# Performance work log

Hardware: AMD Instinct MI355X
Metric: run time of the kernel (lower is better)

## Reference

```python
import jax, jax.numpy as jnp
import numpy as np

ALPHA = 0.3          # triplet margin
LOSS_WEIGHT = 1.0
VALID_COST = 100.0   # chosen so all queries are valid (query2gt ~ U[0,1))
POS_T = 3            # pos_thresh
NEG_T = 30           # neg_thresh
EPS = 1e-6           # torch pairwise_distance eps


def setup_inputs() -> dict:
    key0 = jax.random.key(0)
    ks = jax.random.split(key0, 6)
    Nq, V, K, D, G = 2048, 6, 4096, 256, 64
    attn = jax.random.normal(ks[0], (Nq, V, K), dtype=jnp.float32)
    query2gt = jax.random.uniform(ks[1], (Nq, G), dtype=jnp.float32)  # min < VALID_COST always
    query = jax.random.normal(ks[2], (Nq, V, D), dtype=jnp.float32)
    key = jax.random.normal(ks[3], (K, V, D), dtype=jnp.float32)
    pos_idx = jax.random.randint(ks[4], (V * Nq,), 0, POS_T, dtype=jnp.int64 if jax.config.jax_enable_x64 else jnp.int32)
    neg_idx = jax.random.randint(ks[5], (V * Nq,), POS_T, NEG_T, dtype=jnp.int64 if jax.config.jax_enable_x64 else jnp.int32)
    return {"attn": attn, "query2gt": query2gt, "query": query, "key": key,
            "pos_idx": pos_idx, "neg_idx": neg_idx}


def reference(attn, query2gt, query, key, pos_idx, neg_idx):
    # valid filtering: query2gt.min(-1) < VALID_COST is all-True by construction,
    # so no rows are dropped (keeps shapes static under jit).
    q = jnp.transpose(query, (1, 0, 2))   # [V, Nq, D]
    k = jnp.transpose(key, (1, 0, 2))     # [V, K, D]
    a = jnp.transpose(attn, (1, 0, 2))    # [V, Nq, K]
    V, Nq, K = a.shape

    # batched euclidean cdist per view via gram expansion
    qq = jnp.sum(q * q, axis=-1)[:, :, None]          # [V, Nq, 1]
    kk = jnp.sum(k * k, axis=-1)[:, None, :]          # [V, 1, K]
    d2 = qq + kk - 2.0 * jnp.einsum('vnd,vkd->vnk', q, k)
    dist = jnp.sqrt(jnp.maximum(d2, 0.0))             # [V, Nq, K]

    sorted_idx = jnp.argsort(dist, axis=-1).reshape(V * Nq, K)
    a = a.reshape(V * Nq, K)
    r = jnp.arange(V * Nq)

    pos = jax.nn.sigmoid(a[r, sorted_idx[r, pos_idx]])  # [V*Nq]
    neg = jax.nn.sigmoid(a[r, sorted_idx[r, neg_idx]])  # [V*Nq]

    # TripletMarginLoss(margin=ALPHA, p=1) with anchor = ones, 1-d embeddings
    d_pos = jnp.abs(1.0 - pos + EPS)
    d_neg = jnp.abs(1.0 - neg + EPS)
    loss = jnp.mean(jnp.maximum(d_pos - d_neg + ALPHA, 0.0))
    return LOSS_WEIGHT * loss
```

## Files before the change

### kernel.cpp

```cpp
#include <hip/hip_runtime.h>
#include <stdint.h>

#define NQ    2048
#define VV    6
#define KCNT  4096
#define DD    256
#define NROWS (VV*NQ)
#define ALPHA_M 0.3f
#define EPSL  1e-6f
#define SBIAS 256.0f
#define ZTHR  2.05f
#define CAP   256

#define TM 128
#define TN 128
#define BKK 32

typedef _Float16 f16x8 __attribute__((ext_vector_type(8)));
typedef _Float16 f16x4 __attribute__((ext_vector_type(4)));
typedef float    f32x4 __attribute__((ext_vector_type(4)));

__device__ __forceinline__ void gload16(const void* g, void* l) {
    __builtin_amdgcn_global_load_lds(
        (__attribute__((address_space(1))) void*)(uintptr_t)g,
        (__attribute__((address_space(3))) void*)(uintptr_t)(uint32_t)(uintptr_t)l,
        16, 0, 0);
}

__device__ __forceinline__ unsigned ord16(_Float16 h) {
    unsigned short b = __builtin_bit_cast(unsigned short, h);
    return (b & 0x8000u) ? (unsigned)(~b & 0xFFFFu) : (unsigned)(b | 0x8000u);
}

__device__ __forceinline__ float triplet_term(const float* attn, int r, int kpos, int kneg) {
    int v = r / NQ, q = r - v * NQ;
    float apos = attn[(size_t)q * (VV*KCNT) + v*KCNT + kpos];
    float aneg = attn[(size_t)q * (VV*KCNT) + v*KCNT + kneg];
    float pv = 1.0f / (1.0f + expf(-apos));
    float nv = 1.0f / (1.0f + expf(-aneg));
    float dp = fabsf(1.0f - pv + EPSL);
    float dn = fabsf(1.0f - nv + EPSL);
    return fmaxf(dp - dn + ALPHA_M, 0.0f);
}

__global__ __launch_bounds__(256) void pack_fused(const float* __restrict__ key,
                                                  const float* __restrict__ query,
                                                  _Float16* __restrict__ Bpack,
                                                  _Float16* __restrict__ Apack,
                                                  float* __restrict__ kkp,
                                                  float* __restrict__ Trow,
                                                  unsigned* __restrict__ fcount,
                                                  float* __restrict__ out)
{
    int wid  = threadIdx.x >> 6;
    int lane = threadIdx.x & 63;
    if (blockIdx.x < 6144) {
        int rowid = blockIdx.x * 4 + wid;
        int k = rowid / 6;
        int v = rowid - k * 6;
        float4 x = *(const float4*)(key + (size_t)rowid * DD + lane * 4);
        f16x4 h;
        h.x = (_Float16)x.x; h.y = (_Float16)x.y;
        h.z = (_Float16)x.z; h.w = (_Float16)x.w;
        *(f16x4*)(Bpack + ((size_t)(v * KCNT + k)) * DD + lane * 4) = h;

        float s = x.x*x.x + x.y*x.y + x.z*x.z + x.w*x.w;
        #pragma unroll
        for (int off = 32; off >= 1; off >>= 1) s += __shfl_xor(s, off);
        if (lane == 0) kkp[v * KCNT + k] = s;
    } else {
        int bid2 = blockIdx.x - 6144;
        if (bid2 == 0) {
            if (threadIdx.x == 0) *fcount = 0;
            if (threadIdx.x == 1) out[0] = 0.0f;
        }
        int rowid = bid2 * 4 + wid;
        int q = rowid / 6;
        int v = rowid - q * 6;
        float4 x = *(const float4*)(query + (size_t)rowid * DD + lane * 4);
        f16x4 h;
        h.x = (_Float16)x.x; h.y = (_Float16)x.y;
        h.z = (_Float16)x.z; h.w = (_Float16)x.w;
        *(f16x4*)(Apack + ((size_t)(v * NQ + q)) * DD + lane * 4) = h;

        float qq = x.x*x.x + x.y*x.y + x.z*x.z + x.w*x.w;
        #pragma unroll
        for (int off = 32; off >= 1; off >>= 1) qq += __shfl_xor(qq, off);
        if (lane == 0)
            Trow[v * NQ + q] = 256.0f - ZTHR * sqrtf(512.0f + 4.0f * qq);
    }
}

__global__ __launch_bounds__(256) void score_gemm(const _Float16* __restrict__ Apack,
                                                  const _Float16* __restrict__ Bpack,
                                                  const float* __restrict__ kkp,
                                                  const float* __restrict__ Trow,
                                                  unsigned long long* __restrict__ maskb,
                                                  _Float16* __restrict__ wsf)
{
    __shared__ _Float16 As[TM * BKK];
    __shared__ _Float16 Bs[TN * BKK];

    int tid  = threadIdx.x;
    int wid  = tid >> 6;
    int lane = tid & 63;
    int c0   = blockIdx.x * TN;
    int grow = blockIdx.y * TM;
    int v    = grow / NQ;
    int q0   = grow - v * NQ;

    int srow = (wid << 4) + (lane >> 2);
    int sseg = (lane & 3) ^ ((lane >> 2) & 3);
    const _Float16* Ag0 = Apack + ((size_t)(v*NQ   + q0 + srow)) * DD + sseg*8;
    const _Float16* Ag1 = Ag0 + (size_t)64 * DD;
    const _Float16* Bg0 = Bpack + ((size_t)(v*KCNT + c0 + srow)) * DD + sseg*8;
    const _Float16* Bg1 = Bg0 + (size_t)64 * DD;

    _Float16* lA0 = As + wid*512;
    _Float16* lA1 = As + 2048 + wid*512;
    _Float16* lB0 = Bs + wid*512;
    _Float16* lB1 = Bs + 2048 + wid*512;

    int fr = lane & 15;
    int kg = lane >> 4;
    int rb = (wid >> 1) * 64;
    int cb = (wid & 1) * 64;
    int rg = lane >> 4;
    int ksw = (kg ^ (fr & 3)) << 3;

    f32x4 acc[4][4] = {};

    for (int kb = 0; kb < DD; kb += BKK) {
        __syncthreads();
        gload16(Ag0 + kb, lA0);
        gload16(Ag1 + kb, lA1);
        gload16(Bg0 + kb, lB0);
        gload16(Bg1 + kb, lB1);
        __syncthreads();

        f16x8 af[4], bf[4];
        #pragma unroll
        for (int m = 0; m < 4; ++m)
            af[m] = *(const f16x8*)&As[(rb + m*16 + fr)*BKK + ksw];
        #pragma unroll
        for (int n = 0; n < 4; ++n)
            bf[n] = *(const f16x8*)&Bs[(cb + n*16 + fr)*BKK + ksw];
        #pragma unroll
        for (int m = 0; m < 4; ++m)
            #pragma unroll
            for (int n = 0; n < 4; ++n)
                acc[m][n] = __builtin_amdgcn_mfma_f32_16x16x32_f16(af[m], bf[n], acc[m][n], 0, 0, 0);
    }

    int chunk = blockIdx.x * 2 + (wid & 1);
    float kkv[4];
    #pragma unroll
    for (int n = 0; n < 4; ++n)
        kkv[n] = kkp[v*KCNT + c0 + cb + n*16 + fr];

    int sh = rg * 16;

    #pragma unroll
    for (int m = 0; m < 4; ++m) {
        #pragma unroll
        for (int j = 0; j < 4; ++j) {
            int gr = grow + rb + m*16 + rg*4 + j;
            float Tr = Trow[gr];
            unsigned long long mk = 0;
            #pragma unroll
            for (int n = 0; n < 4; ++n) {
                float s = kkv[n] - 2.0f * acc[m][n][j];
                wsf[(size_t)gr * KCNT + (c0 + cb + n*16 + fr)] = (_Float16)(s - SBIAS);
                unsigned long long bal = __ballot(s < Tr);
                mk |= (unsigned long long)((unsigned)(bal >> sh) & 0xFFFFu) << (n*16);
            }
            if (fr == 0) maskb[((size_t)gr << 6) + chunk] = mk;
        }
    }
}

__global__ __launch_bounds__(256) void select2_kernel(const unsigned long long* __restrict__ maskb,
                                                      const _Float16* __restrict__ wsf,
                                                      const float* __restrict__ attn,
                                                      const int* __restrict__ pos_idx,
                                                      const int* __restrict__ neg_idx,
                                                      unsigned* __restrict__ fcount,
                                                      int* __restrict__ flist,
                                                      float* __restrict__ out)
{
    __shared__ unsigned cbuf[4][CAP];
    __shared__ float bsum;
    if (threadIdx.x == 0) bsum = 0.0f;
    __syncthreads();

    int wid  = threadIdx.x >> 6;
    int lane = threadIdx.x & 63;
    int r    = blockIdx.x * 4 + wid;
    int p = pos_idx[r];
    int n = neg_idx[r];

    unsigned long long mk = maskb[((size_t)r << 6) + lane];
    unsigned c_l = (unsigned)__popcll(mk);
    unsigned pre = c_l;
    #pragma unroll
    for (int off = 1; off <= 32; off <<= 1) {
        unsigned o = __shfl_up(pre, off);
        if (lane >= off) pre += o;
    }
    unsigned total = __shfl(pre, 63);
    unsigned excl  = pre - c_l;

    if (total < (unsigned)(n + 1) || total > CAP) {
        if (lane == 0) {
            unsigned i = atomicAdd(fcount, 1u);
            flist[i] = r;
        }
    } else {
        unsigned* mybuf = cbuf[wid];
        const _Float16* srow = wsf + (size_t)r * KCNT + (lane << 6);
        unsigned idx = excl;
        unsigned long long t = mk;
        while (t) {
            int b = __ffsll((long long)t) - 1;
            t &= t - 1;
            _Float16 h = srow[b];
            mybuf[idx++] = (ord16(h) << 12) | (unsigned)((lane << 6) + b);
        }
        __asm__ volatile("s_waitcnt lgkmcnt(0)" ::: "memory");

        unsigned v0 = (lane       < (int)total) ? mybuf[lane]       : 0xFFFFFFFFu;
        unsigned v1 = (lane + 64  < (int)total) ? mybuf[lane + 64]  : 0xFFFFFFFFu;
        unsigned v2 = (lane + 128 < (int)total) ? mybuf[lane + 128] : 0xFFFFFFFFu;
        unsigned v3 = (lane + 192 < (int)total) ? mybuf[lane + 192] : 0xFFFFFFFFu;
        int kpos = 0, kneg = 0;
        for (int t2 = 0; t2 <= n; ++t2) {
            unsigned m01 = v0 < v1 ? v0 : v1;
            unsigned m23 = v2 < v3 ? v2 : v3;
            unsigned m = m01 < m23 ? m01 : m23;
            #pragma unroll
            for (int off = 32; off >= 1; off >>= 1) {
                unsigned o = __shfl_xor(m, off);
                m = o < m ? o : m;
            }
            if      (v0 == m) v0 = 0xFFFFFFFFu;
            else if (v1 == m) v1 = 0xFFFFFFFFu;
            else if (v2 == m) v2 = 0xFFFFFFFFu;
            else if (v3 == m) v3 = 0xFFFFFFFFu;
            if (t2 == p) kpos = (int)(m & 0xFFFu);
            if (t2 == n) kneg = (int)(m & 0xFFFu);
        }
        if (lane == 0)
            atomicAdd(&bsum, triplet_term(attn, r, kpos, kneg) * (1.0f / (float)NROWS));
    }
    __syncthreads();
    if (threadIdx.x == 0) atomicAdd(out, bsum);
}

__global__ __launch_bounds__(256) void fallback_kernel(const _Float16* __restrict__ Apack,
                                                       const _Float16* __restrict__ Bpack,
                                                       const float* __restrict__ kkp,
                                                       const float* __restrict__ attn,
                                                       const int* __restrict__ pos_idx,
                                                       const int* __restrict__ neg_idx,
                                                       const unsigned* __restrict__ fcount,
                                                       const int* __restrict__ flist,
                                                       float* __restrict__ out)
{
    __shared__ float qrow[DD];
    __shared__ unsigned keys[KCNT];
    int nf = (int)*fcount;
    for (int it = blockIdx.x; it < nf; it += gridDim.x) {
        int r = flist[it];
        int v = r / NQ, q = r - v * NQ;
        qrow[threadIdx.x] = (float)Apack[((size_t)(v*NQ + q)) * DD + threadIdx.x];
        __syncthreads();
        for (int i = 0; i < 16; ++i) {
            int c = i * 256 + threadIdx.x;
            float dot = 0.0f;
            const f16x8* bp = (const f16x8*)(Bpack + ((size_t)(v*KCNT + c)) * DD);
            for (int d8 = 0; d8 < 32; ++d8) {
                f16x8 b = bp[d8];
                #pragma unroll
                for (int j = 0; j < 8; ++j) dot += qrow[d8*8 + j] * (float)b[j];
            }
            float s = kkp[v*KCNT + c] - 2.0f * dot;
            keys[c] = (ord16((_Float16)(s - SBIAS)) << 12) | (unsigned)c;
        }
        __syncthreads();
        if (threadIdx.x < 64) {
            int lane = threadIdx.x;
            int p = pos_idx[r], n = neg_idx[r];
            unsigned prev = 0;
            int kpos = 0, kneg = 0;
            for (int t = 0; t <= n; ++t) {
                unsigned m = 0xFFFFFFFFu;
                for (int i = 0; i < 64; ++i) {
                    unsigned kk2 = keys[i*64 + lane];
                    if (kk2 > prev && kk2 < m) m = kk2;
                }
                #pragma unroll
                for (int off = 32; off >= 1; off >>= 1) {
                    unsigned o = __shfl_xor(m, off);
                    m = o < m ? o : m;
                }
                if (t == p) kpos = (int)(m & 0xFFFu);
                if (t == n) kneg = (int)(m & 0xFFFu);
                prev = m;
            }
            if (lane == 0)
                atomicAdd(out, triplet_term(attn, r, kpos, kneg) * (1.0f / (float)NROWS));
        }
        __syncthreads();
    }
}

extern "C" void kernel_launch(void* const* d_in, const int* in_sizes, int n_in,
                              void* d_out, int out_size, void* d_ws, size_t ws_size,
                              hipStream_t stream)
{
    const float* attn    = (const float*)d_in[0];
    const float* query   = (const float*)d_in[2];
    const float* key     = (const float*)d_in[3];
    const int*   pos_idx = (const int*)d_in[4];
    const int*   neg_idx = (const int*)d_in[5];
    float* out = (float*)d_out;

    char* w = (char*)d_ws;
    unsigned*           fcount = (unsigned*)(w);
    float*              Trow   = (float*)   (w + 256);
    float*              kkp    = (float*)   (w + 49408);
    int*                flist  = (int*)     (w + 147712);
    unsigned long long* maskb  = (unsigned long long*)(w + 196864);
    _Float16*           Apack  = (_Float16*)(w + 6488320);
    _Float16*           Bpack  = (_Float16*)(w + 12779776);
    _Float16*           wsf    = (_Float16*)(w + 25362688);

    pack_fused<<<9216, 256, 0, stream>>>(key, query, Bpack, Apack, kkp, Trow,
                                         fcount, out);

    dim3 gg(KCNT / TN, NROWS / TM);
    score_gemm<<<gg, 256, 0, stream>>>(Apack, Bpack, kkp, Trow, maskb, wsf);

    select2_kernel<<<NROWS / 4, 256, 0, stream>>>(maskb, wsf, attn, pos_idx, neg_idx,
                                                  fcount, flist, out);
    fallback_kernel<<<64, 256, 0, stream>>>(Apack, Bpack, kkp, attn, pos_idx, neg_idx,
                                            fcount, flist, out);
}
```

Baseline: 125.1 us.

## Transpose mask layout via LDS staging and swizzle GEMM block order

The score GEMM now stages each block's 64-bit candidate masks in shared memory and writes them in a chunk-major transposed layout, so the stores are contiguous across threads instead of strided 8-byte writes. The select kernel reads the transposed layout, which makes its per-lane mask loads strided. The GEMM block index is also remapped so consecutive blocks spread across row tiles, aiming for better L2 reuse or XCD spreading. The fallback grid shrinks from 64 to 16 blocks.

```diff
diff --git a/kernel.cpp b/kernel.cpp
--- a/kernel.cpp
+++ b/kernel.cpp
@@ -95,17 +95,24 @@
                                                   const _Float16* __restrict__ Bpack,
                                                   const float* __restrict__ kkp,
                                                   const float* __restrict__ Trow,
-                                                  unsigned long long* __restrict__ maskb,
+                                                  unsigned long long* __restrict__ maskbT,
                                                   _Float16* __restrict__ wsf)
 {
     __shared__ _Float16 As[TM * BKK];
     __shared__ _Float16 Bs[TN * BKK];
+    __shared__ unsigned long long lmask[TM][2];
 
     int tid  = threadIdx.x;
     int wid  = tid >> 6;
     int lane = tid & 63;
-    int c0   = blockIdx.x * TN;
-    int grow = blockIdx.y * TM;
+
+    int fid = blockIdx.y * 32 + blockIdx.x;
+    int swz = (fid & 7) * 384 + (fid >> 3);
+    int bx  = swz & 31;
+    int by  = swz >> 5;
+
+    int c0   = bx * TN;
+    int grow = by * TM;
     int v    = grow / NQ;
     int q0   = grow - v * NQ;
 
@@ -152,7 +159,7 @@
                 acc[m][n] = __builtin_amdgcn_mfma_f32_16x16x32_f16(af[m], bf[n], acc[m][n], 0, 0, 0);
     }
 
-    int chunk = blockIdx.x * 2 + (wid & 1);
+    int cl = wid & 1;
     float kkv[4];
     #pragma unroll
     for (int n = 0; n < 4; ++n)
@@ -164,7 +171,8 @@
     for (int m = 0; m < 4; ++m) {
         #pragma unroll
         for (int j = 0; j < 4; ++j) {
-            int gr = grow + rb + m*16 + rg*4 + j;
+            int lr = rb + m*16 + rg*4 + j;
+            int gr = grow + lr;
             float Tr = Trow[gr];
             unsigned long long mk = 0;
             #pragma unroll
@@ -174,12 +182,18 @@
                 unsigned long long bal = __ballot(s < Tr);
                 mk |= (unsigned long long)((unsigned)(bal >> sh) & 0xFFFFu) << (n*16);
             }
-            if (fr == 0) maskb[((size_t)gr << 6) + chunk] = mk;
-        }
-    }
-}
-
-__global__ __launch_bounds__(256) void select2_kernel(const unsigned long long* __restrict__ maskb,
+            if (fr == 0) lmask[lr][cl] = mk;
+        }
+    }
+    __syncthreads();
+
+    if (tid < TM)
+        maskbT[(size_t)(bx*2 + 0) * NROWS + grow + tid]         = lmask[tid][0];
+    else
+        maskbT[(size_t)(bx*2 + 1) * NROWS + grow + (tid - TM)]  = lmask[tid - TM][1];
+}
+
+__global__ __launch_bounds__(256) void select2_kernel(const unsigned long long* __restrict__ maskbT,
                                                       const _Float16* __restrict__ wsf,
                                                       const float* __restrict__ attn,
                                                       const int* __restrict__ pos_idx,
@@ -199,7 +213,7 @@
     int p = pos_idx[r];
     int n = neg_idx[r];
 
-    unsigned long long mk = maskb[((size_t)r << 6) + lane];
+    unsigned long long mk = maskbT[(size_t)lane * NROWS + r];
     unsigned c_l = (unsigned)__popcll(mk);
     unsigned pre = c_l;
     #pragma unroll
@@ -330,7 +344,7 @@
     float*              Trow   = (float*)   (w + 256);
     float*              kkp    = (float*)   (w + 49408);
     int*                flist  = (int*)     (w + 147712);
-    unsigned long long* maskb  = (unsigned long long*)(w + 196864);
+    unsigned long long* maskbT = (unsigned long long*)(w + 196864);
     _Float16*           Apack  = (_Float16*)(w + 6488320);
     _Float16*           Bpack  = (_Float16*)(w + 12779776);
     _Float16*           wsf    = (_Float16*)(w + 25362688);
@@ -339,10 +353,10 @@
                                          fcount, out);
 
     dim3 gg(KCNT / TN, NROWS / TM);
-    score_gemm<<<gg, 256, 0, stream>>>(Apack, Bpack, kkp, Trow, maskb, wsf);
-
-    select2_kernel<<<NROWS / 4, 256, 0, stream>>>(maskb, wsf, attn, pos_idx, neg_idx,
+    score_gemm<<<gg, 256, 0, stream>>>(Apack, Bpack, kkp, Trow, maskbT, wsf);
+
+    select2_kernel<<<NROWS / 4, 256, 0, stream>>>(maskbT, wsf, attn, pos_idx, neg_idx,
                                                   fcount, flist, out);
-    fallback_kernel<<<64, 256, 0, stream>>>(Apack, Bpack, kkp, attn, pos_idx, neg_idx,
+    fallback_kernel<<<16, 256, 0, stream>>>(Apack, Bpack, kkp, attn, pos_idx, neg_idx,
                                             fcount, flist, out);
 }
```

Result: no change. 125.5 us (+0.4%).
